# Optimization experiments

Measured on AMD Instinct MI355X. Metric: run time of the kernel, lower is better.

The kernel has to match this reference:

```python
import jax, jax.numpy as jnp
import numpy as np

B, N, G, K = 4, 8192, 512, 32          # batch, points, num_group, group_size
D, H, DEPTH, ENC, MLP = 768, 12, 4, 256, 3072
HD = D // H


def _fps(xyz, npoint):
    """Farthest point sampling, starts at index 0 (as pointnet2_utils). xyz: [B,N,3] -> idx [B,npoint]."""
    b, n, _ = xyz.shape
    def step(carry, _):
        dmin, far = carry                                   # dmin [b,n], far [b]
        c = jax.vmap(lambda p, i: p[i])(xyz, far)           # [b,3]
        d = jnp.sum((xyz - c[:, None, :]) ** 2, -1)         # [b,n]
        dmin = jnp.minimum(dmin, d)
        nxt = jnp.argmax(dmin, -1).astype(jnp.int32)
        return (dmin, nxt), far
    init = (jnp.full((b, n), 1e10, jnp.float32), jnp.zeros((b,), jnp.int32))
    _, idx = jax.lax.scan(step, init, None, length=npoint)
    return jnp.transpose(idx)                                # [b, npoint]


def _sqdist(a, b):
    # [B,S,C] x [B,M,C] -> [B,S,M] squared euclidean
    return (jnp.sum(a * a, -1)[:, :, None]
            - 2.0 * jnp.einsum('bsc,bmc->bsm', a, b)
            + jnp.sum(b * b, -1)[:, None, :])


def _bn(x, g, b, m, v):   # eval-mode BatchNorm1d, channels-last
    return (x - m) * jax.lax.rsqrt(v + 1e-5) * g + b


def _ln(x, g, b):
    mu = jnp.mean(x, -1, keepdims=True)
    va = jnp.var(x, -1, keepdims=True)
    return (x - mu) * jax.lax.rsqrt(va + 1e-5) * g + b


def setup_inputs():
    key = jax.random.key(0)
    cnt = [0]
    def rn(shape, s=0.02):
        cnt[0] += 1
        return jax.random.normal(jax.random.fold_in(key, cnt[0]), shape, jnp.float32) * s
    inp = dict(
        pts=jax.random.uniform(jax.random.fold_in(key, 1000), (B, N, 3), jnp.float32),
        colors=jax.random.uniform(jax.random.fold_in(key, 1001), (B, N, 3), jnp.float32),
        enc_w1a=rn((128, 6), 0.2), enc_b1a=rn((128,)),
        bn1_g=jnp.ones((128,)), bn1_b=jnp.zeros((128,)), bn1_m=jnp.zeros((128,)), bn1_v=jnp.ones((128,)),
        enc_w1b=rn((256, 128), 0.05), enc_b1b=rn((256,)),
        enc_w2a=rn((512, 512), 0.03), enc_b2a=rn((512,)),
        bn2_g=jnp.ones((512,)), bn2_b=jnp.zeros((512,)), bn2_m=jnp.zeros((512,)), bn2_v=jnp.ones((512,)),
        enc_w2b=rn((ENC, 512), 0.03), enc_b2b=rn((ENC,)),
        e2t_w=rn((D, ENC), 0.04), e2t_b=rn((D,)),
        cls_token=jnp.zeros((1, 1, D)), cls_pos=rn((1, 1, D), 1.0),
        pe_w1=rn((128, 3), 0.3), pe_b1=rn((128,)),
        pe_w2=rn((D, 128), 0.05), pe_b2=rn((D,)),
        ln1_g=jnp.ones((DEPTH, D)), ln1_b=jnp.zeros((DEPTH, D)),
        qkv_w=rn((DEPTH, D, 3 * D)), qkv_b=rn((DEPTH, 3 * D)),
        proj_w=rn((DEPTH, D, D)), proj_b=rn((DEPTH, D)),
        ln2_g=jnp.ones((DEPTH, D)), ln2_b=jnp.zeros((DEPTH, D)),
        mlp_w1=rn((DEPTH, D, MLP)), mlp_b1=rn((DEPTH, MLP)),
        mlp_w2=rn((DEPTH, MLP, D)), mlp_b2=rn((DEPTH, D)),
        fcn_g=jnp.ones((D,)), fcn_b=jnp.zeros((D,)),
        t2e_w=rn((D, D)), t2e_b=rn((D,)),
    )
    return inp


def reference(pts, colors, enc_w1a, enc_b1a, bn1_g, bn1_b, bn1_m, bn1_v,
              enc_w1b, enc_b1b, enc_w2a, enc_b2a, bn2_g, bn2_b, bn2_m, bn2_v,
              enc_w2b, enc_b2b, e2t_w, e2t_b, cls_token, cls_pos,
              pe_w1, pe_b1, pe_w2, pe_b2,
              ln1_g, ln1_b, qkv_w, qkv_b, proj_w, proj_b,
              ln2_g, ln2_b, mlp_w1, mlp_b1, mlp_w2, mlp_b2,
              fcn_g, fcn_b, t2e_w, t2e_b):
    b = pts.shape[0]
    # ---- Group: FPS centers + kNN grouping ----
    fidx = _fps(pts, G)                                        # [B,G]
    center = jax.vmap(lambda p, i: p[i])(pts, fidx)            # [B,G,3]
    d = _sqdist(center, pts)                                   # [B,G,N]
    _, knn = jax.lax.top_k(-d, K)                              # [B,G,K] smallest dists
    nbr = jax.vmap(lambda p, i: p[i])(pts, knn)                # [B,G,K,3]
    nbr_c = jax.vmap(lambda p, i: p[i])(colors, knn)           # [B,G,K,3]
    nbr = nbr - center[:, :, None, :]
    feat = jnp.concatenate([nbr, nbr_c], -1)                   # [B,G,K,6]
    # ---- mini-PointNet Encoder (conv1d k=1 == linear over channels) ----
    x = feat.reshape(b * G, K, 6)
    f = jax.nn.relu(_bn(x @ enc_w1a.T + enc_b1a, bn1_g, bn1_b, bn1_m, bn1_v))
    f = f @ enc_w1b.T + enc_b1b                                # [M,K,256]
    fg = jnp.max(f, axis=1, keepdims=True)                     # [M,1,256]
    f = jnp.concatenate([jnp.broadcast_to(fg, (b * G, K, 256)), f], -1)  # [M,K,512]
    f = jax.nn.relu(_bn(f @ enc_w2a.T + enc_b2a, bn2_g, bn2_b, bn2_m, bn2_v))
    f = f @ enc_w2b.T + enc_b2b                                # [M,K,ENC]
    tok = jnp.max(f, axis=1).reshape(b, G, ENC)                # [B,G,ENC]
    # ---- to transformer ----
    tok = tok @ e2t_w.T + e2t_b                                # [B,G,D]
    pos = jax.nn.gelu(center @ pe_w1.T + pe_b1, approximate=False) @ pe_w2.T + pe_b2
    xs = jnp.concatenate([jnp.broadcast_to(cls_token, (b, 1, D)), tok], 1)
    ps = jnp.concatenate([jnp.broadcast_to(cls_pos, (b, 1, D)), pos], 1)
    xs = xs + ps                                               # [B,G+1,D]
    s = G + 1
    scale = HD ** -0.5
    for i in range(DEPTH):
        h = _ln(xs, ln1_g[i], ln1_b[i])
        qkv = (h @ qkv_w[i] + qkv_b[i]).reshape(b, s, 3, H, HD)
        q, k, v = qkv[:, :, 0], qkv[:, :, 1], qkv[:, :, 2]
        att = jax.nn.softmax(jnp.einsum('bshd,bthd->bhst', q, k) * scale, -1)
        o = jnp.einsum('bhst,bthd->bshd', att, v).reshape(b, s, D)
        xs = xs + o @ proj_w[i] + proj_b[i]
        h = _ln(xs, ln2_g[i], ln2_b[i])
        h = jax.nn.gelu(h @ mlp_w1[i] + mlp_b1[i], approximate=False) @ mlp_w2[i] + mlp_b2[i]
        xs = xs + h
    xs = _ln(xs, fcn_g, fcn_b)
    return xs @ t2e_w.T + t2e_b                                # [B,G+1,embed_dim]
```

## Files before the change

### kernel.cpp

```cpp
#include <hip/hip_runtime.h>
#include <math.h>

#define BB 4
#define NN 8192
#define GG 512
#define KK 32
#define DD 768
#define SS 513
#define HH 12

typedef __attribute__((ext_vector_type(8))) short bf16x8;
typedef __attribute__((ext_vector_type(4))) float f32x4;

__device__ __forceinline__ float gelu_f(float x) {
  return 0.5f * x * (1.f + erff(x * 0.70710678118654752f));
}
__device__ __forceinline__ unsigned short f2b(float f) {
  unsigned u = __float_as_uint(f);
  u = (u + 0x7FFFu + ((u >> 16) & 1u)) >> 16;
  return (unsigned short)u;
}
__device__ __forceinline__ float b2f(unsigned short h) {
  return __uint_as_float(((unsigned)h) << 16);
}

__global__ __launch_bounds__(1024) void fps_kernel(const float* __restrict__ pts,
                                                   int* __restrict__ fidx,
                                                   float* __restrict__ center) {
  int b = blockIdx.x;
  int tid = threadIdx.x;
  const float* P = pts + (size_t)b * NN * 3;
  float x[8], y[8], z[8], dmin[8];
#pragma unroll
  for (int j = 0; j < 8; j++) {
    int p = tid + 1024 * j;
    x[j] = P[p * 3 + 0]; y[j] = P[p * 3 + 1]; z[j] = P[p * 3 + 2];
    dmin[j] = 1e10f;
  }
  __shared__ unsigned long long sred[16];
  __shared__ int sfar;
  __shared__ float scx, scy, scz;
  int far = 0;
  for (int it = 0; it < GG; it++) {
    if (tid == 0) {
      float cx = P[far * 3 + 0], cy = P[far * 3 + 1], cz = P[far * 3 + 2];
      scx = cx; scy = cy; scz = cz;
      fidx[b * GG + it] = far;
      center[(size_t)(b * GG + it) * 3 + 0] = cx;
      center[(size_t)(b * GG + it) * 3 + 1] = cy;
      center[(size_t)(b * GG + it) * 3 + 2] = cz;
    }
    __syncthreads();
    float cx = scx, cy = scy, cz = scz;
    unsigned long long best = 0;
#pragma unroll
    for (int j = 0; j < 8; j++) {
      float dx = __fsub_rn(x[j], cx);
      float dy = __fsub_rn(y[j], cy);
      float dz = __fsub_rn(z[j], cz);
      float d = __fadd_rn(__fadd_rn(__fmul_rn(dx, dx), __fmul_rn(dy, dy)), __fmul_rn(dz, dz));
      float dm = fminf(dmin[j], d);
      dmin[j] = dm;
      unsigned long long key = ((unsigned long long)__float_as_uint(dm) << 32)
                             | (unsigned)(0xFFFFFFFFu - (unsigned)(tid + 1024 * j));
      best = (key > best) ? key : best;
    }
#pragma unroll
    for (int off = 32; off > 0; off >>= 1) {
      unsigned long long o = __shfl_xor(best, off);
      best = (o > best) ? o : best;
    }
    int lane = tid & 63, wid = tid >> 6;
    if (lane == 0) sred[wid] = best;
    __syncthreads();
    if (tid < 16) {
      unsigned long long v = sred[tid];
#pragma unroll
      for (int off = 8; off > 0; off >>= 1) {
        unsigned long long o = __shfl_xor(v, off);
        v = (o > v) ? o : v;
      }
      if (tid == 0) sfar = (int)(0xFFFFFFFFu - (unsigned)(v & 0xFFFFFFFFu));
    }
    __syncthreads();
    far = sfar;
  }
}

__global__ __launch_bounds__(256) void knn_kernel(const float* __restrict__ pts,
                                                  const float* __restrict__ center,
                                                  int* __restrict__ knn_idx) {
  int bg = blockIdx.x;
  int b = bg >> 9;
  int tid = threadIdx.x;
  __shared__ float dist[NN];
  __shared__ unsigned long long sred[4];
  const float* P = pts + (size_t)b * NN * 3;
  float cx = center[bg * 3 + 0], cy = center[bg * 3 + 1], cz = center[bg * 3 + 2];
  for (int j = 0; j < 32; j++) {
    int p = tid + 256 * j;
    float dx = P[p * 3 + 0] - cx, dy = P[p * 3 + 1] - cy, dz = P[p * 3 + 2] - cz;
    dist[p] = dx * dx + dy * dy + dz * dz;
  }
  __syncthreads();
  for (int r = 0; r < KK; r++) {
    unsigned long long best = 0xFFFFFFFFFFFFFFFFull;
#pragma unroll 8
    for (int j = 0; j < 32; j++) {
      int p = tid + 256 * j;
      unsigned long long key = ((unsigned long long)__float_as_uint(dist[p]) << 32) | (unsigned)p;
      best = (key < best) ? key : best;
    }
#pragma unroll
    for (int off = 32; off > 0; off >>= 1) {
      unsigned long long o = __shfl_xor(best, off);
      best = (o < best) ? o : best;
    }
    int lane = tid & 63, wid = tid >> 6;
    if (lane == 0) sred[wid] = best;
    __syncthreads();
    if (tid < 4) {
      unsigned long long v = sred[tid];
      unsigned long long o = __shfl_xor(v, 1); v = (o < v) ? o : v;
      o = __shfl_xor(v, 2); v = (o < v) ? o : v;
      if (tid == 0) {
        int p = (int)(v & 0xFFFFFFFFu);
        knn_idx[bg * KK + r] = p;
        dist[p] = 3.0e38f;
      }
    }
    __syncthreads();
  }
}

__global__ __launch_bounds__(256) void cvt_kernel(const float* __restrict__ s,
                                                  unsigned short* __restrict__ d, int n) {
  int i = (blockIdx.x * 256 + threadIdx.x) * 4;
  if (i + 3 < n) {
    float4 v = *reinterpret_cast<const float4*>(&s[i]);
    d[i + 0] = f2b(v.x); d[i + 1] = f2b(v.y); d[i + 2] = f2b(v.z); d[i + 3] = f2b(v.w);
  }
}

__global__ __launch_bounds__(256) void tc_kernel(const float* __restrict__ src,
                                                 unsigned short* __restrict__ dst,
                                                 int K, int N) {
  __shared__ float t[32][33];
  int n0 = blockIdx.x * 32, k0 = blockIdx.y * 32;
  int tx = threadIdx.x & 31, ty = threadIdx.x >> 5;
#pragma unroll
  for (int i = 0; i < 32; i += 8)
    t[ty + i][tx] = src[(size_t)(k0 + ty + i) * N + n0 + tx];
  __syncthreads();
#pragma unroll
  for (int i = 0; i < 32; i += 8)
    dst[(size_t)(n0 + ty + i) * K + k0 + tx] = f2b(t[tx][ty + i]);
}

__global__ __launch_bounds__(256) void enc1a_kernel(
    const float* __restrict__ pts, const float* __restrict__ colors,
    const int* __restrict__ knn_idx, const float* __restrict__ center,
    const float* __restrict__ w1a, const float* __restrict__ b1a,
    const float* __restrict__ bn1g, const float* __restrict__ bn1b,
    const float* __restrict__ bn1m, const float* __restrict__ bn1v,
    unsigned short* __restrict__ f1, int gbase)
{
  int g = gbase + blockIdx.x;
  int b = g >> 9;
  int tid = threadIdx.x;
  __shared__ float feat[KK][8];
  if (tid < 192) {
    int k = tid / 6, c = tid % 6;
    int p = knn_idx[g * KK + k];
    float v;
    if (c < 3) v = pts[(size_t)(b * NN + p) * 3 + c] - center[g * 3 + c];
    else       v = colors[(size_t)(b * NN + p) * 3 + (c - 3)];
    feat[k][c] = v;
  }
  __syncthreads();
  for (int e = tid; e < KK * 128; e += 256) {
    int k = e >> 7, j = e & 127;
    float s = b1a[j];
#pragma unroll
    for (int c = 0; c < 6; c++) s += feat[k][c] * w1a[j * 6 + c];
    s = (s - bn1m[j]) * rsqrtf(bn1v[j] + 1e-5f) * bn1g[j] + bn1b[j];
    f1[((size_t)blockIdx.x * KK + k) * 128 + j] = f2b(fmaxf(s, 0.f));
  }
}

__global__ __launch_bounds__(256) void maxpool_kernel(const unsigned short* __restrict__ in,
                                                      unsigned short* __restrict__ out, int total) {
  int e = blockIdx.x * 256 + threadIdx.x;
  if (e >= total) return;
  int g = e >> 8, c = e & 255;
  const unsigned short* p = in + ((size_t)g * 32) * 256 + c;
  float m = -3e38f;
#pragma unroll 8
  for (int k = 0; k < 32; k++) m = fmaxf(m, b2f(p[k * 256]));
  out[e] = f2b(m);
}

template <int ACT, int RESID, int OUTBF, int CONCAT>
__global__ __launch_bounds__(256) void bgemm(
    const unsigned short* __restrict__ A, const unsigned short* __restrict__ fg,
    const unsigned short* __restrict__ W, const float* __restrict__ bias,
    const float* __restrict__ resid, void* __restrict__ outp,
    int M, int N, int K,
    const float* __restrict__ bng, const float* __restrict__ bnb,
    const float* __restrict__ bnm, const float* __restrict__ bnv)
{
  __shared__ unsigned short As[128][40];
  __shared__ unsigned short Bs[128][40];
  const int tid = threadIdx.x;
  const int tm0 = blockIdx.y * 128, tn0 = blockIdx.x * 128;
  const int w = tid >> 6, l = tid & 63;
  const int wr = (w >> 1) * 64, wc = (w & 1) * 64;
  const int lr = l & 15, lk = l >> 4;

  f32x4 zero4 = {0.f, 0.f, 0.f, 0.f};
  f32x4 acc[4][4];
#pragma unroll
  for (int m = 0; m < 4; m++)
#pragma unroll
    for (int n = 0; n < 4; n++) acc[m][n] = zero4;

  for (int k0 = 0; k0 < K; k0 += 32) {
#pragma unroll
    for (int c = 0; c < 2; c++) {
      int s = tid + c * 256;
      int row = s >> 2, kp = s & 3;
      uint4 va = make_uint4(0u, 0u, 0u, 0u);
      int grow = tm0 + row;
      if (grow < M) {
        if (CONCAT) {
          int kk = k0 + kp * 8;
          const unsigned short* src = (kk < 256)
              ? &fg[((size_t)(grow >> 5)) * 256 + kk]
              : &A[(size_t)grow * 256 + (kk - 256)];
          va = *reinterpret_cast<const uint4*>(src);
        } else {
          va = *reinterpret_cast<const uint4*>(&A[(size_t)grow * K + k0 + kp * 8]);
        }
      }
      *reinterpret_cast<uint4*>(&As[row][kp * 8]) = va;
      uint4 vb = *reinterpret_cast<const uint4*>(&W[(size_t)(tn0 + row) * K + k0 + kp * 8]);
      *reinterpret_cast<uint4*>(&Bs[row][kp * 8]) = vb;
    }
    __syncthreads();
    bf16x8 af[4], bfr[4];
#pragma unroll
    for (int m = 0; m < 4; m++)
      af[m] = *reinterpret_cast<const bf16x8*>(&As[wr + m * 16 + lr][lk * 8]);
#pragma unroll
    for (int n = 0; n < 4; n++)
      bfr[n] = *reinterpret_cast<const bf16x8*>(&Bs[wc + n * 16 + lr][lk * 8]);
#pragma unroll
    for (int m = 0; m < 4; m++)
#pragma unroll
      for (int n = 0; n < 4; n++)
        acc[m][n] = __builtin_amdgcn_mfma_f32_16x16x32_bf16(af[m], bfr[n], acc[m][n], 0, 0, 0);
    __syncthreads();
  }
#pragma unroll
  for (int m = 0; m < 4; m++) {
#pragma unroll
    for (int r = 0; r < 4; r++) {
      int row = tm0 + wr + m * 16 + lk * 4 + r;
      if (row >= M) continue;
#pragma unroll
      for (int n = 0; n < 4; n++) {
        int col = tn0 + wc + n * 16 + lr;
        float v = acc[m][n][r] + bias[col];
        if (ACT == 1) v = gelu_f(v);
        if (ACT == 2) {
          v = (v - bnm[col]) * rsqrtf(bnv[col] + 1e-5f) * bng[col] + bnb[col];
          v = fmaxf(v, 0.f);
        }
        if (RESID) v += resid[(size_t)row * N + col];
        if (OUTBF) ((unsigned short*)outp)[(size_t)row * N + col] = f2b(v);
        else       ((float*)outp)[(size_t)row * N + col] = v;
      }
    }
  }
}

template <int TRANSB, int ACT, int RESID>
__global__ __launch_bounds__(256) void gemm_kernel(
    const float* __restrict__ A, const float* __restrict__ W,
    const float* __restrict__ bias, const float* __restrict__ resid,
    float* __restrict__ out, int M, int N, int K)
{
  __shared__ float Asm[16][64];
  __shared__ float Bsm[16][64];
  int tile_n = blockIdx.x * 64, tile_m = blockIdx.y * 64;
  int tid = threadIdx.x;
  int tm = tid >> 4, tn = tid & 15;
  float acc[4][4] = {};
  for (int k0 = 0; k0 < K; k0 += 16) {
    {
      int e = tid * 4;
      int m = e >> 4, k = e & 15;
      int row = tile_m + m;
      float4 v = make_float4(0.f, 0.f, 0.f, 0.f);
      if (row < M) v = *reinterpret_cast<const float4*>(&A[(size_t)row * K + k0 + k]);
      Asm[k + 0][m] = v.x; Asm[k + 1][m] = v.y; Asm[k + 2][m] = v.z; Asm[k + 3][m] = v.w;
    }
    if (TRANSB == 0) {
      int e = tid * 4;
      int n = e & 63, k = e >> 6;
      float4 v = *reinterpret_cast<const float4*>(&W[(size_t)(k0 + k) * N + tile_n + n]);
      *reinterpret_cast<float4*>(&Bsm[k][n]) = v;
    } else {
      int e = tid * 4;
      int k = e & 15, n = e >> 4;
      float4 v = *reinterpret_cast<const float4*>(&W[(size_t)(tile_n + n) * K + k0 + k]);
      Bsm[k + 0][n] = v.x; Bsm[k + 1][n] = v.y; Bsm[k + 2][n] = v.z; Bsm[k + 3][n] = v.w;
    }
    __syncthreads();
#pragma unroll
    for (int kk = 0; kk < 16; kk++) {
      float4 a = *reinterpret_cast<const float4*>(&Asm[kk][tm * 4]);
      float4 wv = *reinterpret_cast<const float4*>(&Bsm[kk][tn * 4]);
      acc[0][0] += a.x * wv.x; acc[0][1] += a.x * wv.y; acc[0][2] += a.x * wv.z; acc[0][3] += a.x * wv.w;
      acc[1][0] += a.y * wv.x; acc[1][1] += a.y * wv.y; acc[1][2] += a.y * wv.z; acc[1][3] += a.y * wv.w;
      acc[2][0] += a.z * wv.x; acc[2][1] += a.z * wv.y; acc[2][2] += a.z * wv.z; acc[2][3] += a.z * wv.w;
      acc[3][0] += a.w * wv.x; acc[3][1] += a.w * wv.y; acc[3][2] += a.w * wv.z; acc[3][3] += a.w * wv.w;
    }
    __syncthreads();
  }
#pragma unroll
  for (int i = 0; i < 4; i++) {
    int row = tile_m + tm * 4 + i;
    if (row >= M) continue;
    int col = tile_n + tn * 4;
    float4 r;
    r.x = acc[i][0] + bias[col + 0];
    r.y = acc[i][1] + bias[col + 1];
    r.z = acc[i][2] + bias[col + 2];
    r.w = acc[i][3] + bias[col + 3];
    if (ACT == 1) { r.x = gelu_f(r.x); r.y = gelu_f(r.y); r.z = gelu_f(r.z); r.w = gelu_f(r.w); }
    if (RESID) {
      float4 rr = *reinterpret_cast<const float4*>(&resid[(size_t)row * N + col]);
      r.x += rr.x; r.y += rr.y; r.z += rr.z; r.w += rr.w;
    }
    *reinterpret_cast<float4*>(&out[(size_t)row * N + col]) = r;
  }
}

template <int OUTBF>
__global__ __launch_bounds__(256) void ln_kernel(const float* __restrict__ x,
                                                 const float* __restrict__ g,
                                                 const float* __restrict__ bta,
                                                 void* __restrict__ yv) {
  int r = blockIdx.x;
  int tid = threadIdx.x;
  __shared__ float sred[4];
  __shared__ float smu, srs;
  const float* xr = x + (size_t)r * 768;
  float v0 = xr[tid], v1 = xr[tid + 256], v2 = xr[tid + 512];
  float s = v0 + v1 + v2;
#pragma unroll
  for (int off = 32; off > 0; off >>= 1) s += __shfl_xor(s, off);
  if ((tid & 63) == 0) sred[tid >> 6] = s;
  __syncthreads();
  if (tid < 4) {
    float t = sred[tid];
    t += __shfl_xor(t, 1); t += __shfl_xor(t, 2);
    if (tid == 0) smu = t * (1.f / 768.f);
  }
  __syncthreads();
  float mu = smu;
  float d0 = v0 - mu, d1 = v1 - mu, d2 = v2 - mu;
  float ss = d0 * d0 + d1 * d1 + d2 * d2;
#pragma unroll
  for (int off = 32; off > 0; off >>= 1) ss += __shfl_xor(ss, off);
  if ((tid & 63) == 0) sred[tid >> 6] = ss;
  __syncthreads();
  if (tid < 4) {
    float t = sred[tid];
    t += __shfl_xor(t, 1); t += __shfl_xor(t, 2);
    if (tid == 0) srs = rsqrtf(t * (1.f / 768.f) + 1e-5f);
  }
  __syncthreads();
  float rs = srs;
  float o0 = d0 * rs * g[tid]       + bta[tid];
  float o1 = d1 * rs * g[tid + 256] + bta[tid + 256];
  float o2 = d2 * rs * g[tid + 512] + bta[tid + 512];
  if (OUTBF) {
    unsigned short* yr = (unsigned short*)yv + (size_t)r * 768;
    yr[tid] = f2b(o0); yr[tid + 256] = f2b(o1); yr[tid + 512] = f2b(o2);
  } else {
    float* yr = (float*)yv + (size_t)r * 768;
    yr[tid] = o0; yr[tid + 256] = o1; yr[tid + 512] = o2;
  }
}

__global__ __launch_bounds__(256) void pe_hidden_kernel(const float* __restrict__ center,
                                                        const float* __restrict__ w1,
                                                        const float* __restrict__ b1,
                                                        float* __restrict__ hid) {
  int e = blockIdx.x * 256 + threadIdx.x;
  int r = e >> 7, j = e & 127;
  float cx = center[r * 3 + 0], cy = center[r * 3 + 1], cz = center[r * 3 + 2];
  float s = b1[j] + cx * w1[j * 3 + 0] + cy * w1[j * 3 + 1] + cz * w1[j * 3 + 2];
  hid[e] = gelu_f(s);
}

__global__ __launch_bounds__(256) void assemble_kernel(const float* __restrict__ tp,
                                                       const float* __restrict__ pp,
                                                       const float* __restrict__ cls_tok,
                                                       const float* __restrict__ cls_pos,
                                                       float* __restrict__ xs) {
  int r = blockIdx.x;
  int b = r / SS, t = r % SS;
  int tid = threadIdx.x;
  float* xr = xs + (size_t)r * 768;
  if (t == 0) {
    for (int d = tid; d < 768; d += 256) xr[d] = cls_tok[d] + cls_pos[d];
  } else {
    int g = b * GG + (t - 1);
    for (int d = tid; d < 768; d += 256) xr[d] = tp[(size_t)g * 768 + d] + pp[(size_t)g * 768 + d];
  }
}

__global__ __launch_bounds__(256) void flash_kernel(const float* __restrict__ qkv,
                                                    unsigned short* __restrict__ o) {
  int qt = blockIdx.x, h = blockIdx.y, b = blockIdx.z;
  int tid = threadIdx.x;
  int rr = tid >> 2, cg = tid & 3;
  __shared__ float Ks[64][68];
  __shared__ float Vs[64][68];
  __shared__ float Ps[64][68];
  const float scale = 0.125f;
  int qrow = qt * 64 + rr;
  bool qvalid = qrow < SS;
  float q[16];
  {
    const float* qp = qkv + (size_t)(b * SS + (qvalid ? qrow : 0)) * 2304 + h * 64 + cg * 16;
#pragma unroll
    for (int i = 0; i < 16; i += 4) {
      float4 v = *reinterpret_cast<const float4*>(qp + i);
      q[i + 0] = qvalid ? v.x * scale : 0.f;
      q[i + 1] = qvalid ? v.y * scale : 0.f;
      q[i + 2] = qvalid ? v.z * scale : 0.f;
      q[i + 3] = qvalid ? v.w * scale : 0.f;
    }
  }
  float O[16];
#pragma unroll
  for (int i = 0; i < 16; i++) O[i] = 0.f;
  float mrow = -3e38f, lrow = 0.f;
  for (int kc = 0; kc < 9; kc++) {
    int kbase = kc * 64;
    for (int e = tid; e < 64 * 64; e += 256) {
      int krow = e >> 6, d = e & 63;
      int gk = kbase + krow;
      float kv = 0.f, vv = 0.f;
      if (gk < SS) {
        const float* pk = qkv + (size_t)(b * SS + gk) * 2304 + 768 + h * 64 + d;
        kv = *pk; vv = pk[768];
      }
      Ks[krow][d] = kv; Vs[krow][d] = vv;
    }
    __syncthreads();
    float svals[16];
    float mc = -3e38f;
    for (int kk = 0; kk < 64; kk++) {
      const float* kr = &Ks[kk][cg * 16];
      float p = 0.f;
#pragma unroll
      for (int i = 0; i < 16; i++) p += q[i] * kr[i];
      p += __shfl_xor(p, 1);
      p += __shfl_xor(p, 2);
      float s = (kbase + kk < SS) ? p : -3e38f;
      if ((kk & 3) == cg) svals[kk >> 2] = s;
      mc = fmaxf(mc, s);
    }
    float mnew = fmaxf(mrow, mc);
    float alpha = __expf(mrow - mnew);
    float lsum = 0.f;
#pragma unroll
    for (int jj = 0; jj < 16; jj++) {
      float pexp = __expf(svals[jj] - mnew);
      lsum += pexp;
      Ps[rr][jj * 4 + cg] = pexp;
    }
    lsum += __shfl_xor(lsum, 1);
    lsum += __shfl_xor(lsum, 2);
    lrow = lrow * alpha + lsum;
#pragma unroll
    for (int i = 0; i < 16; i++) O[i] *= alpha;
    mrow = mnew;
    __syncthreads();
#pragma unroll 4
    for (int kk = 0; kk < 64; kk++) {
      float pw = Ps[rr][kk];
      const float* vr = &Vs[kk][cg * 16];
#pragma unroll
      for (int i = 0; i < 16; i++) O[i] += pw * vr[i];
    }
    __syncthreads();
  }
  if (qvalid) {
    float inv = 1.f / lrow;
    unsigned short* op = o + (size_t)(b * SS + qrow) * 768 + h * 64 + cg * 16;
#pragma unroll
    for (int i = 0; i < 16; i++) op[i] = f2b(O[i] * inv);
  }
}

extern "C" void kernel_launch(void* const* d_in, const int* in_sizes, int n_in,
                              void* d_out, int out_size, void* d_ws, size_t ws_size,
                              hipStream_t stream) {
  const float* pts    = (const float*)d_in[0];
  const float* colors = (const float*)d_in[1];
  const float* w1a    = (const float*)d_in[2];
  const float* b1a    = (const float*)d_in[3];
  const float* bn1g   = (const float*)d_in[4];
  const float* bn1b   = (const float*)d_in[5];
  const float* bn1m   = (const float*)d_in[6];
  const float* bn1v   = (const float*)d_in[7];
  const float* w1b    = (const float*)d_in[8];
  const float* b1b    = (const float*)d_in[9];
  const float* w2a    = (const float*)d_in[10];
  const float* b2a    = (const float*)d_in[11];
  const float* bn2g   = (const float*)d_in[12];
  const float* bn2b   = (const float*)d_in[13];
  const float* bn2m   = (const float*)d_in[14];
  const float* bn2v   = (const float*)d_in[15];
  const float* w2b    = (const float*)d_in[16];
  const float* b2b    = (const float*)d_in[17];
  const float* e2t_w  = (const float*)d_in[18];
  const float* e2t_b  = (const float*)d_in[19];
  const float* cls_token = (const float*)d_in[20];
  const float* cls_pos   = (const float*)d_in[21];
  const float* pe_w1  = (const float*)d_in[22];
  const float* pe_b1  = (const float*)d_in[23];
  const float* pe_w2  = (const float*)d_in[24];
  const float* pe_b2  = (const float*)d_in[25];
  const float* ln1_g  = (const float*)d_in[26];
  const float* ln1_b  = (const float*)d_in[27];
  const float* qkv_w  = (const float*)d_in[28];
  const float* qkv_b  = (const float*)d_in[29];
  const float* proj_w = (const float*)d_in[30];
  const float* proj_b = (const float*)d_in[31];
  const float* ln2_g  = (const float*)d_in[32];
  const float* ln2_b  = (const float*)d_in[33];
  const float* mlp_w1 = (const float*)d_in[34];
  const float* mlp_b1 = (const float*)d_in[35];
  const float* mlp_w2 = (const float*)d_in[36];
  const float* mlp_b2 = (const float*)d_in[37];
  const float* fcn_g  = (const float*)d_in[38];
  const float* fcn_b  = (const float*)d_in[39];
  const float* t2e_w  = (const float*)d_in[40];
  const float* t2e_b  = (const float*)d_in[41];

  if (ws_size < (size_t)67174400) return;

  char* ws = (char*)d_ws;
  int*            fidx   = (int*)(ws + 0);
  float*          center = (float*)(ws + 8192);
  int*            knn    = (int*)(ws + 32768);
  unsigned short* tok    = (unsigned short*)(ws + 294912);
  float*          xs     = (float*)(ws + 1343488);
  unsigned short* hbuf   = (unsigned short*)(ws + 7647232);
  float*          fbuf   = (float*)(ws + 10799104);
  char*           WT     = ws + 17102848;
  unsigned short* qkv_wt = (unsigned short*)(WT + 0);
  unsigned short* proj_wt= (unsigned short*)(WT + 3538944);
  unsigned short* w1t    = (unsigned short*)(WT + 4718592);
  unsigned short* w2t    = (unsigned short*)(WT + 9437184);
  unsigned short* w1bb   = (unsigned short*)(WT + 14155776);
  unsigned short* w2ab   = (unsigned short*)(WT + 14221312);
  unsigned short* w2bb   = (unsigned short*)(WT + 14745600);
  unsigned short* e2tb   = (unsigned short*)(WT + 15007744);
  char*           BA     = ws + 32503808;
  unsigned short* f1   = (unsigned short*)(BA + 0);
  unsigned short* f2   = (unsigned short*)(BA + 4194304);
  unsigned short* fg   = (unsigned short*)(BA + 12582912);
  unsigned short* f3   = (unsigned short*)(BA + 12845056);
  unsigned short* f4   = (unsigned short*)(BA + 0);
  float*          tp   = (float*)(BA + 0);
  float*          pp   = (float*)(BA + 6291456);
  float*          hid  = (float*)(BA + 12582912);
  float*          qkvb = (float*)(BA + 0);
  unsigned short* obuf = (unsigned short*)(BA + 18911232);
  unsigned short* mh   = (unsigned short*)(BA + 22063104);

  cvt_kernel<<<32, 256, 0, stream>>>(w1b, w1bb, 32768);
  cvt_kernel<<<256, 256, 0, stream>>>(w2a, w2ab, 262144);
  cvt_kernel<<<128, 256, 0, stream>>>(w2b, w2bb, 131072);
  cvt_kernel<<<192, 256, 0, stream>>>(e2t_w, e2tb, 196608);

  fps_kernel<<<BB, 1024, 0, stream>>>(pts, fidx, center);
  knn_kernel<<<BB * GG, 256, 0, stream>>>(pts, center, knn);

  for (int c = 0; c < 4; c++) {
    int gbase = c * 512;
    enc1a_kernel<<<512, 256, 0, stream>>>(pts, colors, knn, center,
        w1a, b1a, bn1g, bn1b, bn1m, bn1v, f1, gbase);
    bgemm<0, 0, 1, 0><<<dim3(2, 128), 256, 0, stream>>>(f1, nullptr, w1bb, b1b,
        nullptr, f2, 16384, 256, 128, nullptr, nullptr, nullptr, nullptr);
    maxpool_kernel<<<512, 256, 0, stream>>>(f2, fg, 512 * 256);
    bgemm<2, 0, 1, 1><<<dim3(4, 128), 256, 0, stream>>>(f2, fg, w2ab, b2a,
        nullptr, f3, 16384, 512, 512, bn2g, bn2b, bn2m, bn2v);
    bgemm<0, 0, 1, 0><<<dim3(2, 128), 256, 0, stream>>>(f3, nullptr, w2bb, b2b,
        nullptr, f4, 16384, 256, 512, nullptr, nullptr, nullptr, nullptr);
    maxpool_kernel<<<512, 256, 0, stream>>>(f4, tok + (size_t)gbase * 256, 512 * 256);
  }

  bgemm<0, 0, 0, 0><<<dim3(6, 16), 256, 0, stream>>>(tok, nullptr, e2tb, e2t_b,
      nullptr, tp, 2048, 768, 256, nullptr, nullptr, nullptr, nullptr);
  pe_hidden_kernel<<<1024, 256, 0, stream>>>(center, pe_w1, pe_b1, hid);
  gemm_kernel<1, 0, 0><<<dim3(12, 32), 256, 0, stream>>>(hid, pe_w2, pe_b2, nullptr, pp, 2048, 768, 128);
  assemble_kernel<<<BB * SS, 256, 0, stream>>>(tp, pp, cls_token, cls_pos, xs);

  for (int i = 0; i < 4; i++) {
    tc_kernel<<<dim3(72, 24), 256, 0, stream>>>(qkv_w + (size_t)i * 768 * 2304, qkv_wt, 768, 2304);
    tc_kernel<<<dim3(24, 24), 256, 0, stream>>>(proj_w + (size_t)i * 768 * 768, proj_wt, 768, 768);
    tc_kernel<<<dim3(96, 24), 256, 0, stream>>>(mlp_w1 + (size_t)i * 768 * 3072, w1t, 768, 3072);
    tc_kernel<<<dim3(24, 96), 256, 0, stream>>>(mlp_w2 + (size_t)i * 3072 * 768, w2t, 3072, 768);

    ln_kernel<1><<<BB * SS, 256, 0, stream>>>(xs, ln1_g + i * 768, ln1_b + i * 768, hbuf);
    bgemm<0, 0, 0, 0><<<dim3(18, 17), 256, 0, stream>>>(hbuf, nullptr, qkv_wt,
        qkv_b + i * 2304, nullptr, qkvb, 2052, 2304, 768, nullptr, nullptr, nullptr, nullptr);
    flash_kernel<<<dim3(9, 12, 4), 256, 0, stream>>>(qkvb, obuf);
    bgemm<0, 1, 0, 0><<<dim3(6, 17), 256, 0, stream>>>(obuf, nullptr, proj_wt,
        proj_b + i * 768, xs, xs, 2052, 768, 768, nullptr, nullptr, nullptr, nullptr);
    ln_kernel<1><<<BB * SS, 256, 0, stream>>>(xs, ln2_g + i * 768, ln2_b + i * 768, hbuf);
    bgemm<1, 0, 1, 0><<<dim3(24, 17), 256, 0, stream>>>(hbuf, nullptr, w1t,
        mlp_b1 + i * 3072, nullptr, mh, 2052, 3072, 768, nullptr, nullptr, nullptr, nullptr);
    bgemm<0, 1, 0, 0><<<dim3(6, 17), 256, 0, stream>>>(mh, nullptr, w2t,
        mlp_b2 + i * 768, xs, xs, 2052, 768, 3072, nullptr, nullptr, nullptr, nullptr);
  }

  ln_kernel<0><<<BB * SS, 256, 0, stream>>>(xs, fcn_g, fcn_b, fbuf);
  gemm_kernel<1, 0, 0><<<dim3(12, 33), 256, 0, stream>>>(fbuf, t2e_w, t2e_b, nullptr,
      (float*)d_out, 2052, 768, 768);
}
```

Measured before the change: 2.982 ms.

## Streamline FPS reduction with DPP wave ops and restructure flash QK dot products

Farthest point sampling now runs 512 threads per batch, each holding 16 points. The argmax uses DPP-based 32-bit wave max/min reductions followed by a single shared atomicMax. The winning wave writes the next center directly, which removes the 64-bit shuffle tree, the second-level reduction and one barrier per iteration. In the attention kernel each thread now holds the full 64-wide query and computes whole dot products for its own subset of keys. This replaces the cross-lane shuffle sums, K/V tiles load as float4, and the barrier between the softmax write and the P·V read is dropped. The trade-offs are higher register pressure in flash and reliance on Ps being written and read only by lanes of the same wave.

```diff
diff --git a/kernel.cpp b/kernel.cpp
--- a/kernel.cpp
+++ b/kernel.cpp
@@ -24,66 +24,84 @@
   return __uint_as_float(((unsigned)h) << 16);
 }
 
-__global__ __launch_bounds__(1024) void fps_kernel(const float* __restrict__ pts,
-                                                   int* __restrict__ fidx,
-                                                   float* __restrict__ center) {
+__device__ __forceinline__ unsigned wave_max_u32(unsigned v) {
+  unsigned t;
+  t = (unsigned)__builtin_amdgcn_update_dpp(0, (int)v, 0x111, 0xf, 0xf, false); v = t > v ? t : v;
+  t = (unsigned)__builtin_amdgcn_update_dpp(0, (int)v, 0x112, 0xf, 0xf, false); v = t > v ? t : v;
+  t = (unsigned)__builtin_amdgcn_update_dpp(0, (int)v, 0x114, 0xf, 0xf, false); v = t > v ? t : v;
+  t = (unsigned)__builtin_amdgcn_update_dpp(0, (int)v, 0x118, 0xf, 0xf, false); v = t > v ? t : v;
+  t = (unsigned)__builtin_amdgcn_update_dpp(0, (int)v, 0x142, 0xf, 0xf, false); v = t > v ? t : v;
+  t = (unsigned)__builtin_amdgcn_update_dpp(0, (int)v, 0x143, 0xf, 0xf, false); v = t > v ? t : v;
+  return (unsigned)__builtin_amdgcn_readlane((int)v, 63);
+}
+__device__ __forceinline__ unsigned wave_min_u32(unsigned v) {
+  unsigned t;
+  t = (unsigned)__builtin_amdgcn_update_dpp(0x7FFFFFFF, (int)v, 0x111, 0xf, 0xf, false); v = t < v ? t : v;
+  t = (unsigned)__builtin_amdgcn_update_dpp(0x7FFFFFFF, (int)v, 0x112, 0xf, 0xf, false); v = t < v ? t : v;
+  t = (unsigned)__builtin_amdgcn_update_dpp(0x7FFFFFFF, (int)v, 0x114, 0xf, 0xf, false); v = t < v ? t : v;
+  t = (unsigned)__builtin_amdgcn_update_dpp(0x7FFFFFFF, (int)v, 0x118, 0xf, 0xf, false); v = t < v ? t : v;
+  t = (unsigned)__builtin_amdgcn_update_dpp(0x7FFFFFFF, (int)v, 0x142, 0xf, 0xf, false); v = t < v ? t : v;
+  t = (unsigned)__builtin_amdgcn_update_dpp(0x7FFFFFFF, (int)v, 0x143, 0xf, 0xf, false); v = t < v ? t : v;
+  return (unsigned)__builtin_amdgcn_readlane((int)v, 63);
+}
+
+__global__ __launch_bounds__(512) void fps_kernel(const float* __restrict__ pts,
+                                                  int* __restrict__ fidx,
+                                                  float* __restrict__ center) {
   int b = blockIdx.x;
   int tid = threadIdx.x;
   const float* P = pts + (size_t)b * NN * 3;
-  float x[8], y[8], z[8], dmin[8];
-#pragma unroll
-  for (int j = 0; j < 8; j++) {
-    int p = tid + 1024 * j;
+  float x[16], y[16], z[16], dmin[16];
+#pragma unroll
+  for (int j = 0; j < 16; j++) {
+    int p = tid + 512 * j;
     x[j] = P[p * 3 + 0]; y[j] = P[p * 3 + 1]; z[j] = P[p * 3 + 2];
     dmin[j] = 1e10f;
   }
-  __shared__ unsigned long long sred[16];
-  __shared__ int sfar;
+  __shared__ unsigned long long sbest;
   __shared__ float scx, scy, scz;
-  int far = 0;
-  for (int it = 0; it < GG; it++) {
-    if (tid == 0) {
-      float cx = P[far * 3 + 0], cy = P[far * 3 + 1], cz = P[far * 3 + 2];
-      scx = cx; scy = cy; scz = cz;
-      fidx[b * GG + it] = far;
-      center[(size_t)(b * GG + it) * 3 + 0] = cx;
-      center[(size_t)(b * GG + it) * 3 + 1] = cy;
-      center[(size_t)(b * GG + it) * 3 + 2] = cz;
-    }
-    __syncthreads();
+  if (tid == 0) {
+    sbest = 0ull;
+    scx = x[0]; scy = y[0]; scz = z[0];
+    fidx[b * GG] = 0;
+    center[(size_t)(b * GG) * 3 + 0] = x[0];
+    center[(size_t)(b * GG) * 3 + 1] = y[0];
+    center[(size_t)(b * GG) * 3 + 2] = z[0];
+  }
+  __syncthreads();
+  for (int it = 0; it < GG - 1; it++) {
     float cx = scx, cy = scy, cz = scz;
-    unsigned long long best = 0;
-#pragma unroll
-    for (int j = 0; j < 8; j++) {
+    unsigned bv = 0u, bi = 0x7FFFFFFFu;
+    int bj = 0;
+#pragma unroll
+    for (int j = 0; j < 16; j++) {
       float dx = __fsub_rn(x[j], cx);
       float dy = __fsub_rn(y[j], cy);
       float dz = __fsub_rn(z[j], cz);
       float d = __fadd_rn(__fadd_rn(__fmul_rn(dx, dx), __fmul_rn(dy, dy)), __fmul_rn(dz, dz));
       float dm = fminf(dmin[j], d);
       dmin[j] = dm;
-      unsigned long long key = ((unsigned long long)__float_as_uint(dm) << 32)
-                             | (unsigned)(0xFFFFFFFFu - (unsigned)(tid + 1024 * j));
-      best = (key > best) ? key : best;
-    }
-#pragma unroll
-    for (int off = 32; off > 0; off >>= 1) {
-      unsigned long long o = __shfl_xor(best, off);
-      best = (o > best) ? o : best;
-    }
-    int lane = tid & 63, wid = tid >> 6;
-    if (lane == 0) sred[wid] = best;
-    __syncthreads();
-    if (tid < 16) {
-      unsigned long long v = sred[tid];
-#pragma unroll
-      for (int off = 8; off > 0; off >>= 1) {
-        unsigned long long o = __shfl_xor(v, off);
-        v = (o > v) ? o : v;
+      unsigned db = __float_as_uint(dm);
+      if (db > bv) { bv = db; bi = (unsigned)(tid + 512 * j); bj = j; }
+    }
+    unsigned wmax = wave_max_u32(bv);
+    unsigned cand = (bv == wmax) ? bi : 0x7FFFFFFFu;
+    unsigned widx = wave_min_u32(cand);
+    bool wave_winner = (bv == wmax) && (bi == widx);
+    unsigned long long mykey = ((unsigned long long)wmax << 32) | (unsigned long long)(0xFFFFFFFFu - widx);
+    if (wave_winner) atomicMax(&sbest, mykey);
+    __syncthreads();
+    if (wave_winner) {
+      if (sbest == mykey) {
+        scx = x[bj]; scy = y[bj]; scz = z[bj];
+        fidx[b * GG + it + 1] = (int)bi;
+        center[(size_t)(b * GG + it + 1) * 3 + 0] = x[bj];
+        center[(size_t)(b * GG + it + 1) * 3 + 1] = y[bj];
+        center[(size_t)(b * GG + it + 1) * 3 + 2] = z[bj];
+        sbest = 0ull;
       }
-      if (tid == 0) sfar = (int)(0xFFFFFFFFu - (unsigned)(v & 0xFFFFFFFFu));
-    }
-    __syncthreads();
-    far = sfar;
+    }
+    __syncthreads();
   }
 }
 
@@ -434,11 +452,11 @@
   const float scale = 0.125f;
   int qrow = qt * 64 + rr;
   bool qvalid = qrow < SS;
-  float q[16];
+  float q[64];
   {
-    const float* qp = qkv + (size_t)(b * SS + (qvalid ? qrow : 0)) * 2304 + h * 64 + cg * 16;
-#pragma unroll
-    for (int i = 0; i < 16; i += 4) {
+    const float* qp = qkv + (size_t)(b * SS + (qvalid ? qrow : 0)) * 2304 + h * 64;
+#pragma unroll
+    for (int i = 0; i < 64; i += 4) {
       float4 v = *reinterpret_cast<const float4*>(qp + i);
       q[i + 0] = qvalid ? v.x * scale : 0.f;
       q[i + 1] = qvalid ? v.y * scale : 0.f;
@@ -452,30 +470,41 @@
   float mrow = -3e38f, lrow = 0.f;
   for (int kc = 0; kc < 9; kc++) {
     int kbase = kc * 64;
-    for (int e = tid; e < 64 * 64; e += 256) {
-      int krow = e >> 6, d = e & 63;
+#pragma unroll
+    for (int e = tid; e < 1024; e += 256) {
+      int krow = e >> 4, d0 = (e & 15) * 4;
       int gk = kbase + krow;
-      float kv = 0.f, vv = 0.f;
+      float4 kv = make_float4(0.f, 0.f, 0.f, 0.f);
+      float4 vv = make_float4(0.f, 0.f, 0.f, 0.f);
       if (gk < SS) {
-        const float* pk = qkv + (size_t)(b * SS + gk) * 2304 + 768 + h * 64 + d;
-        kv = *pk; vv = pk[768];
+        const float* pk = qkv + (size_t)(b * SS + gk) * 2304 + 768 + h * 64 + d0;
+        kv = *reinterpret_cast<const float4*>(pk);
+        vv = *reinterpret_cast<const float4*>(pk + 768);
       }
-      Ks[krow][d] = kv; Vs[krow][d] = vv;
+      *reinterpret_cast<float4*>(&Ks[krow][d0]) = kv;
+      *reinterpret_cast<float4*>(&Vs[krow][d0]) = vv;
     }
     __syncthreads();
     float svals[16];
     float mc = -3e38f;
-    for (int kk = 0; kk < 64; kk++) {
-      const float* kr = &Ks[kk][cg * 16];
-      float p = 0.f;
-#pragma unroll
-      for (int i = 0; i < 16; i++) p += q[i] * kr[i];
-      p += __shfl_xor(p, 1);
-      p += __shfl_xor(p, 2);
+#pragma unroll 4
+    for (int jj = 0; jj < 16; jj++) {
+      int kk = jj * 4 + cg;
+      const float* kr = &Ks[kk][0];
+      float p0 = 0.f, p1 = 0.f, p2 = 0.f, p3 = 0.f;
+#pragma unroll
+      for (int i = 0; i < 64; i += 4) {
+        float4 kv4 = *reinterpret_cast<const float4*>(kr + i);
+        p0 += q[i + 0] * kv4.x; p1 += q[i + 1] * kv4.y;
+        p2 += q[i + 2] * kv4.z; p3 += q[i + 3] * kv4.w;
+      }
+      float p = (p0 + p1) + (p2 + p3);
       float s = (kbase + kk < SS) ? p : -3e38f;
-      if ((kk & 3) == cg) svals[kk >> 2] = s;
+      svals[jj] = s;
       mc = fmaxf(mc, s);
     }
+    mc = fmaxf(mc, __shfl_xor(mc, 1));
+    mc = fmaxf(mc, __shfl_xor(mc, 2));
     float mnew = fmaxf(mrow, mc);
     float alpha = __expf(mrow - mnew);
     float lsum = 0.f;
@@ -491,7 +520,6 @@
 #pragma unroll
     for (int i = 0; i < 16; i++) O[i] *= alpha;
     mrow = mnew;
-    __syncthreads();
 #pragma unroll 4
     for (int kk = 0; kk < 64; kk++) {
       float pw = Ps[rr][kk];
@@ -592,7 +620,7 @@
   cvt_kernel<<<128, 256, 0, stream>>>(w2b, w2bb, 131072);
   cvt_kernel<<<192, 256, 0, stream>>>(e2t_w, e2tb, 196608);
 
-  fps_kernel<<<BB, 1024, 0, stream>>>(pts, fidx, center);
+  fps_kernel<<<BB, 512, 0, stream>>>(pts, fidx, center);
   knn_kernel<<<BB * GG, 256, 0, stream>>>(pts, center, knn);
 
   for (int c = 0; c < 4; c++) {
```

After: 2.736 ms. 1.09x faster.
